# Kernel tuning notes

Hardware: AMD Instinct MI355X
Metric: run time of the kernel (lower is better)

The kernel has to match this reference:

```python
import jax, jax.numpy as jnp
import numpy as np

N = 10000      # nodes
E = 160000     # edges (before self loops)
F_IN = 512     # in_features
F_OUT = 256    # out_features
SLOPE = 0.2    # LeakyReLU negative slope (PyG GATConv default)
EPS = 1e-12    # F.normalize eps


def setup_inputs() -> dict:
    key = jax.random.key(0)
    ks = jax.random.split(key, 14)
    feat = jax.random.normal(ks[0], (N, F_IN), jnp.float32)
    feat_a = jax.random.normal(ks[1], (N, F_IN), jnp.float32)
    edge_index = jax.random.randint(ks[2], (2, E), 0, N, dtype=jnp.int32)
    # binary neighborhood mask; diagonal set so every row has >=1 entry
    gn = (jax.random.uniform(ks[3], (N, N)) < 0.0016).astype(jnp.float32)
    graph_neigh = gn.at[jnp.arange(N), jnp.arange(N)].set(1.0)
    s1 = 1.0 / np.sqrt(F_IN)
    s2 = 1.0 / np.sqrt(F_OUT)
    return {
        "feat": feat,
        "feat_a": feat_a,
        "edge_index": edge_index,
        "graph_neigh": graph_neigh,
        # conv1: GATConv(F_IN -> F_OUT, heads=1)
        "W1": jax.random.normal(ks[4], (F_OUT, F_IN), jnp.float32) * s1,
        "att_src1": jax.random.normal(ks[5], (F_OUT,), jnp.float32) * s2,
        "att_dst1": jax.random.normal(ks[6], (F_OUT,), jnp.float32) * s2,
        "b1": jnp.zeros((F_OUT,), jnp.float32),
        # conv2: GATConv(F_OUT -> F_IN, heads=1)
        "W2": jax.random.normal(ks[7], (F_IN, F_OUT), jnp.float32) * s2,
        "att_src2": jax.random.normal(ks[8], (F_IN,), jnp.float32) * s1,
        "att_dst2": jax.random.normal(ks[9], (F_IN,), jnp.float32) * s1,
        "b2": jnp.zeros((F_IN,), jnp.float32),
        # discriminator bilinear
        "Wd": jax.random.normal(ks[10], (F_OUT, F_OUT), jnp.float32) * s2,
        "bd": jnp.zeros((), jnp.float32),
    }


def _gat_conv(x, src, dst, W, a_src, a_dst, b):
    # PyG GATConv, heads=1, concat=True, add_self_loops already applied.
    h = x @ W.T                       # [N, out]
    a_s = h @ a_src                   # [N]
    a_d = h @ a_dst                   # [N]
    e = a_s[src] + a_d[dst]           # [E+N]
    e = jnp.where(e > 0, e, SLOPE * e)  # leaky relu
    m = jax.ops.segment_max(e, dst, num_segments=N)
    p = jnp.exp(e - m[dst])
    s = jax.ops.segment_sum(p, dst, num_segments=N)
    coef = p / s[dst]                 # per-dst softmax over incoming edges
    out = jax.ops.segment_sum(coef[:, None] * h[src], dst, num_segments=N)
    return out + b


def reference(feat, feat_a, edge_index, graph_neigh, W1, att_src1, att_dst1, b1,
              W2, att_src2, att_dst2, b2, Wd, bd):
    loops = jnp.arange(N, dtype=edge_index.dtype)
    src = jnp.concatenate([edge_index[0], loops])
    dst = jnp.concatenate([edge_index[1], loops])

    z = _gat_conv(feat, src, dst, W1, att_src1, att_dst1, b1)      # [N, F_OUT]
    hiden_emb = z
    h = _gat_conv(z, src, dst, W2, att_src2, att_dst2, b2)         # [N, F_IN]
    emb = jax.nn.relu(z)
    z_a = _gat_conv(feat_a, src, dst, W1, att_src1, att_dst1, b1)
    emb_a = jax.nn.relu(z_a)

    def readout(e):
        vsum = graph_neigh @ e                                     # [N, F_OUT]
        row_sum = graph_neigh.sum(axis=1, keepdims=True)
        g = vsum / row_sum
        g = g / jnp.maximum(jnp.linalg.norm(g, axis=1, keepdims=True), EPS)
        return jax.nn.sigmoid(g)

    g = readout(emb)
    g_a = readout(emb_a)

    def bilin(x1, x2):
        return jnp.einsum('nd,de,ne->n', x1, Wd, x2)[:, None] + bd

    ret = jnp.concatenate([bilin(emb, g), bilin(emb_a, g)], axis=1)      # [N, 2]
    ret_a = jnp.concatenate([bilin(emb_a, g_a), bilin(emb, g_a)], axis=1)
    return (hiden_emb, h, ret, ret_a)
```

## Files before the change

kernel.cpp:

```cpp
#include <hip/hip_runtime.h>


#define N_NODES 10000
#define F_IN    512
#define F_OUT   256
#define SLOPE   0.2f
#define BCAP    64

typedef unsigned short ushort_t;
typedef __attribute__((ext_vector_type(8))) short short8;
typedef __attribute__((ext_vector_type(4))) float f32x4;

__device__ __forceinline__ float bf2f(ushort_t h) {
    union { unsigned u; float f; } v;
    v.u = ((unsigned)h) << 16;
    return v.f;
}
__device__ __forceinline__ ushort_t f2bf(float f) {
    union { float f; unsigned u; } v; v.f = f;
    unsigned r = v.u + 0x7FFFu + ((v.u >> 16) & 1u);
    return (ushort_t)(r >> 16);
}

#define NF (N_NODES * 512)
#define NW1 (512 * 256)
#define NW2 (512 * 256)
#define NWD (256 * 256)

__global__ __launch_bounds__(256) void cvt_all(const float* __restrict__ feat,
                                               const float* __restrict__ feat_a,
                                               const float* __restrict__ W1,
                                               const float* __restrict__ W2,
                                               const float* __restrict__ Wd,
                                               ushort_t* __restrict__ featbf,
                                               ushort_t* __restrict__ W1bf,
                                               ushort_t* __restrict__ W2bf,
                                               ushort_t* __restrict__ Wdbf,
                                               uint4* __restrict__ zbase, int zu4) {
    int q = blockIdx.x * 256 + threadIdx.x;
    const int total = (2 * NF + NW1 + NW2 + NWD) / 4;
    if (q >= total) {
        int zi = q - total;
        if (zi < zu4) zbase[zi] = make_uint4(0, 0, 0, 0);
        return;
    }
    int i = q * 4;
    const float* s; ushort_t* d;
    if (i < NF)               { s = feat   + i;                 d = featbf + i; }
    else if (i < 2 * NF)      { s = feat_a + (i - NF);          d = featbf + i; }
    else if (i < 2 * NF + NW1){ s = W1 + (i - 2 * NF);          d = W1bf + (i - 2 * NF); }
    else if (i < 2 * NF + NW1 + NW2) { s = W2 + (i - 2 * NF - NW1); d = W2bf + (i - 2 * NF - NW1); }
    else                      { s = Wd + (i - 2 * NF - NW1 - NW2); d = Wdbf + (i - 2 * NF - NW1 - NW2); }
    float4 v = *(const float4*)s;
    uint2 r;
    r.x = (unsigned)f2bf(v.x) | ((unsigned)f2bf(v.y) << 16);
    r.y = (unsigned)f2bf(v.z) | ((unsigned)f2bf(v.w) << 16);
    *(uint2*)d = r;
}

#define BM 64
#define BN 64
#define BK 32
#define MT1 157
#define MT2 313

__device__ __forceinline__ void gemm_bt_dev(ushort_t* As, ushort_t* Bs,
        int bx, int by,
        const ushort_t* __restrict__ A, const ushort_t* __restrict__ B,
        ushort_t* __restrict__ C, int M, int Nn, int K,
        const float* __restrict__ asrc, const float* __restrict__ adst,
        float* __restrict__ as_out, float* __restrict__ ad_out) {
    int m0 = bx * BM;
    int n0 = by * BN;
    int tid = threadIdx.x;
    int wave = tid >> 6, lane = tid & 63;
    int quad = lane >> 4, r16 = lane & 15;

    f32x4 acc[4] = {};

    int srow = tid >> 2;
    int schunk = tid & 3;
    int a_row = m0 + srow; if (a_row >= M) a_row = M - 1;
    int swz = (schunk ^ (srow & 3)) * 8;
    const ushort_t* Ag = A + (size_t)a_row * K + swz;
    const ushort_t* Bg = B + (size_t)(n0 + srow) * K + swz;
#if __has_builtin(__builtin_amdgcn_global_load_lds)
    ushort_t* dA = As + wave * 512;
    ushort_t* dB = Bs + wave * 512;
#endif

    for (int k0 = 0; k0 < K; k0 += BK) {
#if __has_builtin(__builtin_amdgcn_global_load_lds)
        __syncthreads();
        __builtin_amdgcn_global_load_lds(
            (const __attribute__((address_space(1))) void*)(Ag + k0),
            (__attribute__((address_space(3))) void*)dA, 16, 0, 0);
        __builtin_amdgcn_global_load_lds(
            (const __attribute__((address_space(1))) void*)(Bg + k0),
            (__attribute__((address_space(3))) void*)dB, 16, 0, 0);
        __syncthreads();
#else
        uint4 av = *(const uint4*)(Ag + k0);
        uint4 bv = *(const uint4*)(Bg + k0);
        __syncthreads();
        *(uint4*)&As[srow * BK + ((schunk ^ (srow & 3)) * 8)] = av;
        *(uint4*)&Bs[srow * BK + ((schunk ^ (srow & 3)) * 8)] = bv;
        __syncthreads();
#endif
        int am = wave * 16 + r16;
        short8 a = *(const short8*)&As[am * BK + ((quad ^ (am & 3)) * 8)];
#pragma unroll
        for (int i = 0; i < 4; i++) {
            int bn = i * 16 + r16;
            short8 b = *(const short8*)&Bs[bn * BK + ((quad ^ (bn & 3)) * 8)];
            acc[i] = __builtin_amdgcn_mfma_f32_16x16x32_bf16(a, b, acc[i], 0, 0, 0);
        }
    }
    int m_base = m0 + wave * 16 + quad * 4;
#pragma unroll
    for (int i = 0; i < 4; i++) {
        int n = n0 + i * 16 + r16;
#pragma unroll
        for (int r = 0; r < 4; r++) {
            int m = m_base + r;
            if (m < M) C[(size_t)m * Nn + n] = f2bf(acc[i][r]);
        }
    }
    if (as_out) {
        float a0 = asrc[n0 + r16],      d0 = adst[n0 + r16];
        float a1 = asrc[n0 + 16 + r16], d1 = adst[n0 + 16 + r16];
        float a2 = asrc[n0 + 32 + r16], d2 = adst[n0 + 32 + r16];
        float a3 = asrc[n0 + 48 + r16], d3 = adst[n0 + 48 + r16];
#pragma unroll
        for (int r = 0; r < 4; r++) {
            float s  = acc[0][r] * a0 + acc[1][r] * a1 + acc[2][r] * a2 + acc[3][r] * a3;
            float dd = acc[0][r] * d0 + acc[1][r] * d1 + acc[2][r] * d2 + acc[3][r] * d3;
#pragma unroll
            for (int off = 1; off < 16; off <<= 1) {
                s  += __shfl_xor(s, off);
                dd += __shfl_xor(dd, off);
            }
            int m = m_base + r;
            if (r16 == 0 && m < M) {
                atomicAdd(&as_out[m], s);
                atomicAdd(&ad_out[m], dd);
            }
        }
    }
}

template<int NV>
__device__ __forceinline__ void accum_row(float wgt, const ushort_t* p, float* acc) {
    if constexpr (NV == 4) {
        uint2 u = *(const uint2*)p;
        acc[0] += wgt * bf2f((ushort_t)(u.x & 0xFFFFu));
        acc[1] += wgt * bf2f((ushort_t)(u.x >> 16));
        acc[2] += wgt * bf2f((ushort_t)(u.y & 0xFFFFu));
        acc[3] += wgt * bf2f((ushort_t)(u.y >> 16));
    } else {
        uint4 u = *(const uint4*)p;
        acc[0] += wgt * bf2f((ushort_t)(u.x & 0xFFFFu));
        acc[1] += wgt * bf2f((ushort_t)(u.x >> 16));
        acc[2] += wgt * bf2f((ushort_t)(u.y & 0xFFFFu));
        acc[3] += wgt * bf2f((ushort_t)(u.y >> 16));
        acc[4] += wgt * bf2f((ushort_t)(u.z & 0xFFFFu));
        acc[5] += wgt * bf2f((ushort_t)(u.z >> 16));
        acc[6] += wgt * bf2f((ushort_t)(u.w & 0xFFFFu));
        acc[7] += wgt * bf2f((ushort_t)(u.w >> 16));
    }
}

template<int NV>
__device__ __forceinline__ void store_bf(ushort_t* dst, const float* z, bool relu) {
    unsigned rp[NV / 2];
#pragma unroll
    for (int k = 0; k < NV; k += 2) {
        float x = relu ? fmaxf(z[k], 0.f) : z[k];
        float y = relu ? fmaxf(z[k + 1], 0.f) : z[k + 1];
        rp[k / 2] = (unsigned)f2bf(x) | ((unsigned)f2bf(y) << 16);
    }
    if constexpr (NV == 4) {
        *(uint2*)dst = make_uint2(rp[0], rp[1]);
    } else {
        *(uint4*)dst = make_uint4(rp[0], rp[1], rp[2], rp[3]);
    }
}

template<int FF>
__device__ __forceinline__ void row_conv_dev(int w,
        const int* __restrict__ cnt, const int* __restrict__ buckets,
        const float* __restrict__ a_s, const float* __restrict__ a_d,
        const ushort_t* __restrict__ h, const float* __restrict__ bias,
        int nfirst,
        float* __restrict__ out0, ushort_t* __restrict__ outZ,
        ushort_t* __restrict__ outB, ushort_t* __restrict__ out1) {
    constexpr int NV = FF / 64;
    int lane = threadIdx.x & 63;
    int sel = (w >= nfirst) ? 1 : 0;
    int n = w - sel * nfirst;
    size_t roff = (size_t)sel * (size_t)nfirst;
    int deg = min(cnt[n], BCAP);
    float adn = a_d[roff + n];

    float acc[NV];
#pragma unroll
    for (int k = 0; k < NV; k++) acc[k] = 0.f;

    int cv = 0; float e = -1e30f;
    if (lane < deg) {
        cv = buckets[n * BCAP + lane];
        float t = a_s[roff + cv] + adn;
        e = t > 0.f ? t : SLOPE * t;
    }
    float m = e;
#pragma unroll
    for (int off = 32; off; off >>= 1) m = fmaxf(m, __shfl_xor(m, off));
    float wv = (lane < deg) ? expf(e - m) : 0.f;
    float ls = wv;
#pragma unroll
    for (int off = 32; off; off >>= 1) ls += __shfl_xor(ls, off);
    float inv_s = ls > 0.f ? 1.f / ls : 0.f;
    int j = 0;
    for (; j + 3 < deg; j += 4) {
        float w0 = __shfl(wv, j),     w1 = __shfl(wv, j + 1);
        float w2 = __shfl(wv, j + 2), w3 = __shfl(wv, j + 3);
        int   q0 = __shfl(cv, j),     q1 = __shfl(cv, j + 1);
        int   q2 = __shfl(cv, j + 2), q3 = __shfl(cv, j + 3);
        accum_row<NV>(w0, h + (size_t)(roff + q0) * FF + lane * NV, acc);
        accum_row<NV>(w1, h + (size_t)(roff + q1) * FF + lane * NV, acc);
        accum_row<NV>(w2, h + (size_t)(roff + q2) * FF + lane * NV, acc);
        accum_row<NV>(w3, h + (size_t)(roff + q3) * FF + lane * NV, acc);
    }
    for (; j < deg; j++) {
        float wj = __shfl(wv, j);
        int   qj = __shfl(cv, j);
        accum_row<NV>(wj, h + (size_t)(roff + qj) * FF + lane * NV, acc);
    }

    float z[NV];
#pragma unroll
    for (int k = 0; k < NV; k++) z[k] = acc[k] * inv_s + bias[lane * NV + k];

    size_t obase = (size_t)n * FF + lane * NV;
    if (sel == 0) {
        if (out0) {
#pragma unroll
            for (int k = 0; k < NV; k += 4)
                *(float4*)(out0 + obase + k) = make_float4(z[k], z[k+1], z[k+2], z[k+3]);
        }
        if (outZ) store_bf<NV>(outZ + obase, z, false);
        if (outB) store_bf<NV>(outB + obase, z, true);
    } else {
        if (out1) store_bf<NV>(out1 + obase, z, true);
    }
}

template<int FF>
__global__ __launch_bounds__(256) void row_conv_w(const int* __restrict__ cnt,
                                                  const int* __restrict__ buckets,
                                                  const float* __restrict__ a_s,
                                                  const float* __restrict__ a_d,
                                                  const ushort_t* __restrict__ h,
                                                  const float* __restrict__ bias,
                                                  int nfirst, int ntot,
                                                  float* __restrict__ out0,
                                                  ushort_t* __restrict__ outZ,
                                                  ushort_t* __restrict__ outB,
                                                  ushort_t* __restrict__ out1) {
    int w = blockIdx.x * 4 + (threadIdx.x >> 6);
    if (w >= ntot) return;
    row_conv_dev<FF>(w, cnt, buckets, a_s, a_d, h, bias, nfirst, out0, outZ, outB, out1);
}

#define RCAP 256

__device__ __forceinline__ void readout_dev(int nbase, char* smemraw,
        const float* __restrict__ gn,
        const ushort_t* __restrict__ embB, const ushort_t* __restrict__ embA,
        ushort_t* __restrict__ g, ushort_t* __restrict__ ga) {
    int wid = threadIdx.x >> 6, lane = threadIdx.x & 63;
    int n = nbase + wid;
    int (*lists)[RCAP] = (int(*)[RCAP])smemraw;
    int* cnts = (int*)(smemraw + 4 * RCAP * 4);
    if (lane == 0) cnts[wid] = 0;
    __syncthreads();
    const uint4* rowp = (const uint4*)(gn + (size_t)n * N_NODES);
    const int NU4 = N_NODES / 4;
    for (int idx = lane; idx < NU4; idx += 64) {
        uint4 v = rowp[idx];
        if (v.x & 0x7FFFFFFFu) { int p = atomicAdd(&cnts[wid], 1); if (p < RCAP) lists[wid][p] = idx * 4; }
        if (v.y & 0x7FFFFFFFu) { int p = atomicAdd(&cnts[wid], 1); if (p < RCAP) lists[wid][p] = idx * 4 + 1; }
        if (v.z & 0x7FFFFFFFu) { int p = atomicAdd(&cnts[wid], 1); if (p < RCAP) lists[wid][p] = idx * 4 + 2; }
        if (v.w & 0x7FFFFFFFu) { int p = atomicAdd(&cnts[wid], 1); if (p < RCAP) lists[wid][p] = idx * 4 + 3; }
    }
    __syncthreads();
    int c = min(cnts[wid], RCAP);
    float a0[4] = {}, a1[4] = {};
    int j = 0;
    for (; j + 3 < c; j += 4) {
        int i0 = lists[wid][j],     i1 = lists[wid][j + 1];
        int i2 = lists[wid][j + 2], i3 = lists[wid][j + 3];
        accum_row<4>(1.f, embB + (size_t)i0 * 256 + lane * 4, a0);
        accum_row<4>(1.f, embB + (size_t)i1 * 256 + lane * 4, a0);
        accum_row<4>(1.f, embB + (size_t)i2 * 256 + lane * 4, a0);
        accum_row<4>(1.f, embB + (size_t)i3 * 256 + lane * 4, a0);
        accum_row<4>(1.f, embA + (size_t)i0 * 256 + lane * 4, a1);
        accum_row<4>(1.f, embA + (size_t)i1 * 256 + lane * 4, a1);
        accum_row<4>(1.f, embA + (size_t)i2 * 256 + lane * 4, a1);
        accum_row<4>(1.f, embA + (size_t)i3 * 256 + lane * 4, a1);
    }
    for (; j < c; j++) {
        int node = lists[wid][j];
        accum_row<4>(1.f, embB + (size_t)node * 256 + lane * 4, a0);
        accum_row<4>(1.f, embA + (size_t)node * 256 + lane * 4, a1);
    }
    float inv = 1.f / (float)(c > 0 ? c : 1);
    float u0[4], u1[4];
    float s0 = 0.f, s1 = 0.f;
#pragma unroll
    for (int k = 0; k < 4; k++) {
        u0[k] = a0[k] * inv; s0 += u0[k] * u0[k];
        u1[k] = a1[k] * inv; s1 += u1[k] * u1[k];
    }
#pragma unroll
    for (int off = 32; off; off >>= 1) {
        s0 += __shfl_xor(s0, off);
        s1 += __shfl_xor(s1, off);
    }
    float r0 = 1.f / fmaxf(sqrtf(s0), 1e-12f);
    float r1 = 1.f / fmaxf(sqrtf(s1), 1e-12f);
    float go[4], gao[4];
#pragma unroll
    for (int k = 0; k < 4; k++) {
        go[k]  = 1.f / (1.f + expf(-u0[k] * r0));
        gao[k] = 1.f / (1.f + expf(-u1[k] * r1));
    }
    store_bf<4>(g  + (size_t)n * 256 + lane * 4, go,  false);
    store_bf<4>(ga + (size_t)n * 256 + lane * 4, gao, false);
}

#define G1B (MT2 * 4)

__global__ __launch_bounds__(256) void k_conv1(const ushort_t* __restrict__ featbf,
                                               const ushort_t* __restrict__ W1bf,
                                               ushort_t* __restrict__ h1cat,
                                               const float* __restrict__ asrc1,
                                               const float* __restrict__ adst1,
                                               float* __restrict__ as1cat,
                                               float* __restrict__ ad1cat,
                                               const int* __restrict__ src,
                                               const int* __restrict__ dst,
                                               int E, int* cnt, int* buckets) {
    __shared__ __align__(16) ushort_t As[BM * BK];
    __shared__ __align__(16) ushort_t Bs[BN * BK];
    int b = blockIdx.x;
    if (b < G1B) {
        gemm_bt_dev(As, Bs, b % MT2, b / MT2, featbf, W1bf, h1cat,
                    2 * N_NODES, F_OUT, F_IN, asrc1, adst1, as1cat, ad1cat);
    } else {
        int i = (b - G1B) * 256 + (int)threadIdx.x;
        if (i < E) {
            int d = dst[i];
            d = d < 0 ? 0 : (d >= N_NODES ? N_NODES - 1 : d);
            int s = src[i];
            s = s < 0 ? 0 : (s >= N_NODES ? N_NODES - 1 : s);
            int p = atomicAdd(&cnt[d], 1);
            if (p < BCAP) buckets[d * BCAP + p] = s;
        } else if (i < E + N_NODES) {
            int v = i - E;
            int p = atomicAdd(&cnt[v], 1);
            if (p < BCAP) buckets[v * BCAP + p] = v;
        }
    }
}

#define RO_BLOCKS 2500
#define G2B (MT1 * 8)

__global__ __launch_bounds__(256) void k_stage2(const ushort_t* __restrict__ zbf,
                                                const ushort_t* __restrict__ W2bf,
                                                ushort_t* __restrict__ h2,
                                                const float* __restrict__ asrc2,
                                                const float* __restrict__ adst2,
                                                float* __restrict__ as2,
                                                float* __restrict__ ad2,
                                                const float* __restrict__ gn,
                                                const ushort_t* __restrict__ embB,
                                                const ushort_t* __restrict__ embA,
                                                ushort_t* __restrict__ g,
                                                ushort_t* __restrict__ ga) {
    __shared__ __align__(16) char smem[2 * BM * BK * 2];
    int b = blockIdx.x;
    if (b < RO_BLOCKS) {
        readout_dev(b * 4, smem, gn, embB, embA, g, ga);
    } else {
        int bb = b - RO_BLOCKS;
        gemm_bt_dev((ushort_t*)smem, (ushort_t*)smem + BM * BK, bb % MT1, bb / MT1,
                    zbf, W2bf, h2, N_NODES, F_IN, F_OUT, asrc2, adst2, as2, ad2);
    }
}

__global__ __launch_bounds__(256) void k_stage3(const int* __restrict__ cnt,
                                                const int* __restrict__ buckets,
                                                const float* __restrict__ as2,
                                                const float* __restrict__ ad2,
                                                const ushort_t* __restrict__ h2,
                                                const float* __restrict__ b2,
                                                float* __restrict__ out_h,
                                                const ushort_t* __restrict__ Gcat,
                                                const ushort_t* __restrict__ Wdbf,
                                                ushort_t* __restrict__ R2) {
    __shared__ __align__(16) ushort_t As[BM * BK];
    __shared__ __align__(16) ushort_t Bs[BN * BK];
    int b = blockIdx.x;
    if (b < RO_BLOCKS) {
        int w = b * 4 + ((int)threadIdx.x >> 6);
        row_conv_dev<512>(w, cnt, buckets, as2, ad2, h2, b2, N_NODES,
                          out_h, nullptr, nullptr, nullptr);
    } else {
        int bb = b - RO_BLOCKS;
        gemm_bt_dev(As, Bs, bb % MT2, bb / MT2, Gcat, Wdbf, R2,
                    2 * N_NODES, 256, 256, nullptr, nullptr, nullptr, nullptr);
    }
}

__global__ __launch_bounds__(256) void bilin_kernel(const float* __restrict__ z,
                                                    const ushort_t* __restrict__ embA,
                                                    const ushort_t* __restrict__ Q,
                                                    const ushort_t* __restrict__ Qa,
                                                    const float* __restrict__ bdp,
                                                    float* __restrict__ ret,
                                                    float* __restrict__ ret_a) {
    int row = blockIdx.x * 4 + (threadIdx.x >> 6);
    int lane = threadIdx.x & 63;
    if (row >= N_NODES) return;
    const float*    zr = z    + (size_t)row * 256;
    const ushort_t* er = embA + (size_t)row * 256;
    const ushort_t* q  = Q    + (size_t)row * 256;
    const ushort_t* qa = Qa   + (size_t)row * 256;
    float d00 = 0, d01 = 0, d10 = 0, d11 = 0;
    for (int d = lane; d < 256; d += 64) {
        float em = fmaxf(zr[d], 0.f);
        float ea = bf2f(er[d]);
        float qv = bf2f(q[d]), qav = bf2f(qa[d]);
        d00 += em * qv;
        d01 += ea * qv;
        d10 += ea * qav;
        d11 += em * qav;
    }
    for (int off = 32; off; off >>= 1) {
        d00 += __shfl_down(d00, off);
        d01 += __shfl_down(d01, off);
        d10 += __shfl_down(d10, off);
        d11 += __shfl_down(d11, off);
    }
    if (lane == 0) {
        float bd = bdp[0];
        ret[row * 2]       = d00 + bd;
        ret[row * 2 + 1]   = d01 + bd;
        ret_a[row * 2]     = d10 + bd;
        ret_a[row * 2 + 1] = d11 + bd;
    }
}

extern "C" void kernel_launch(void* const* d_in, const int* in_sizes, int n_in,
                              void* d_out, int out_size, void* d_ws, size_t ws_size,
                              hipStream_t stream) {
    const float* feat    = (const float*)d_in[0];
    const float* feat_a  = (const float*)d_in[1];
    const int*   eidx    = (const int*)d_in[2];
    const float* gn      = (const float*)d_in[3];
    const float* W1      = (const float*)d_in[4];
    const float* asrc1   = (const float*)d_in[5];
    const float* adst1   = (const float*)d_in[6];
    const float* b1      = (const float*)d_in[7];
    const float* W2      = (const float*)d_in[8];
    const float* asrc2   = (const float*)d_in[9];
    const float* adst2   = (const float*)d_in[10];
    const float* b2      = (const float*)d_in[11];
    const float* Wd      = (const float*)d_in[12];
    const float* bd      = (const float*)d_in[13];

    const int N = N_NODES;
    const int E = in_sizes[2] / 2;
    const int* src = eidx;
    const int* dst = eidx + E;

    float* out_z    = (float*)d_out;
    float* out_h    = out_z + (size_t)N * F_OUT;
    float* out_ret  = out_h + (size_t)N * F_IN;
    float* out_reta = out_ret + (size_t)N * 2;

    size_t off = 0;
    char* wsb = (char*)d_ws;
    auto carve = [&](size_t bytes) -> void* {
        void* p = wsb + off;
        off = (off + bytes + 255) & ~(size_t)255;
        return p;
    };
    ushort_t* R1     = (ushort_t*)carve((size_t)2 * N * 256 * 2);
    ushort_t* R2     = (ushort_t*)carve((size_t)2 * N * 256 * 2);
    ushort_t* Gcat   = (ushort_t*)carve((size_t)2 * N * 256 * 2);
    ushort_t* embA   = (ushort_t*)carve((size_t)N * 256 * 2);
    ushort_t* embB   = (ushort_t*)carve((size_t)N * 256 * 2);
    ushort_t* zbf    = (ushort_t*)carve((size_t)N * 256 * 2);
    ushort_t* featbf = (ushort_t*)carve((size_t)2 * N * 512 * 2);
    ushort_t* W1bf   = (ushort_t*)carve((size_t)NW1 * 2);
    ushort_t* W2bf   = (ushort_t*)carve((size_t)NW2 * 2);
    ushort_t* Wdbf   = (ushort_t*)carve((size_t)NWD * 2);
    size_t zstart = off;
    float* as1cat = (float*)carve((size_t)2 * N * 4);
    float* ad1cat = (float*)carve((size_t)2 * N * 4);
    float* as2    = (float*)carve((size_t)N * 4);
    float* ad2    = (float*)carve((size_t)N * 4);
    int*   cnt    = (int*)carve((size_t)N * 4);
    size_t zend = off;
    int*   buckets = (int*)carve((size_t)N * BCAP * 4);

    ushort_t* h1cat = R1;
    ushort_t* h2    = R1;
    ushort_t* Qb    = R2;
    ushort_t* Qab   = R2 + (size_t)N * 256;

    const int cvt_total = (2 * NF + NW1 + NW2 + NWD) / 4;
    const int zu4 = (int)((zend - zstart) / 16);
    cvt_all<<<(cvt_total + zu4 + 255) / 256, 256, 0, stream>>>(
        feat, feat_a, W1, W2, Wd, featbf, W1bf, W2bf, Wdbf,
        (uint4*)(wsb + zstart), zu4);

    const int bucketBlocks = (E + N + 255) / 256;
    k_conv1<<<G1B + bucketBlocks, 256, 0, stream>>>(featbf, W1bf, h1cat,
                                                    asrc1, adst1, as1cat, ad1cat,
                                                    src, dst, E, cnt, buckets);

    row_conv_w<256><<<2 * N / 4, 256, 0, stream>>>(cnt, buckets, as1cat, ad1cat, h1cat, b1,
                                                   N, 2 * N, out_z, zbf, embB, embA);

    k_stage2<<<RO_BLOCKS + G2B, 256, 0, stream>>>(zbf, W2bf, h2, asrc2, adst2, as2, ad2,
                                                  gn, embB, embA, Gcat, Gcat + (size_t)N * 256);

    k_stage3<<<RO_BLOCKS + G1B, 256, 0, stream>>>(cnt, buckets, as2, ad2, h2, b2, out_h,
                                                  Gcat, Wdbf, R2);

    bilin_kernel<<<(N + 3) / 4, 256, 0, stream>>>(out_z, embA, Qb, Qab, bd, out_ret, out_reta);
}
```

Measured before the change: 682.9 us.

## Fuse bilinear discriminator into Wd GEMM epilogue and drop bilin kernel

Result: no change. 679.1 us (-0.6%).

```diff
diff --git a/kernel.cpp b/kernel.cpp
--- a/kernel.cpp
+++ b/kernel.cpp
@@ -36,12 +36,15 @@
                                                ushort_t* __restrict__ W1bf,
                                                ushort_t* __restrict__ W2bf,
                                                ushort_t* __restrict__ Wdbf,
-                                               uint4* __restrict__ zbase, int zu4) {
+                                               uint4* __restrict__ zbase, int zu4,
+                                               uint4* __restrict__ zbase2, int zu4b) {
     int q = blockIdx.x * 256 + threadIdx.x;
     const int total = (2 * NF + NW1 + NW2 + NWD) / 4;
     if (q >= total) {
         int zi = q - total;
-        if (zi < zu4) zbase[zi] = make_uint4(0, 0, 0, 0);
+        if (zi < zu4) { zbase[zi] = make_uint4(0, 0, 0, 0); return; }
+        int zi2 = zi - zu4;
+        if (zi2 < zu4b) zbase2[zi2] = make_uint4(0, 0, 0, 0);
         return;
     }
     int i = q * 4;
@@ -69,7 +72,13 @@
         const ushort_t* __restrict__ A, const ushort_t* __restrict__ B,
         ushort_t* __restrict__ C, int M, int Nn, int K,
         const float* __restrict__ asrc, const float* __restrict__ adst,
-        float* __restrict__ as_out, float* __restrict__ ad_out) {
+        float* __restrict__ as_out, float* __restrict__ ad_out,
+        const ushort_t* __restrict__ embB_ = nullptr,
+        const ushort_t* __restrict__ embA_ = nullptr,
+        float* __restrict__ ret = nullptr,
+        float* __restrict__ ret_a = nullptr,
+        const float* __restrict__ bdp = nullptr,
+        int nfirst = 0) {
     int m0 = bx * BM;
     int n0 = by * BN;
     int tid = threadIdx.x;
@@ -117,13 +126,15 @@
         }
     }
     int m_base = m0 + wave * 16 + quad * 4;
-#pragma unroll
-    for (int i = 0; i < 4; i++) {
-        int n = n0 + i * 16 + r16;
-#pragma unroll
-        for (int r = 0; r < 4; r++) {
-            int m = m_base + r;
-            if (m < M) C[(size_t)m * Nn + n] = f2bf(acc[i][r]);
+    if (C) {
+#pragma unroll
+        for (int i = 0; i < 4; i++) {
+            int n = n0 + i * 16 + r16;
+#pragma unroll
+            for (int r = 0; r < 4; r++) {
+                int m = m_base + r;
+                if (m < M) C[(size_t)m * Nn + n] = f2bf(acc[i][r]);
+            }
         }
     }
     if (as_out) {
@@ -144,6 +155,37 @@
             if (r16 == 0 && m < M) {
                 atomicAdd(&as_out[m], s);
                 atomicAdd(&ad_out[m], dd);
+            }
+        }
+    }
+    if (ret) {
+        float bd = (n0 == 0) ? bdp[0] : 0.f;
+#pragma unroll
+        for (int r = 0; r < 4; r++) {
+            int m = m_base + r;
+            int isA = (m >= nfirst) ? 1 : 0;
+            int mm = m - isA * nfirst;
+            float db = 0.f, da = 0.f;
+#pragma unroll
+            for (int i = 0; i < 4; i++) {
+                int c = n0 + i * 16 + r16;
+                float qv = acc[i][r];
+                db += qv * bf2f(embB_[(size_t)mm * 256 + c]);
+                da += qv * bf2f(embA_[(size_t)mm * 256 + c]);
+            }
+#pragma unroll
+            for (int off = 1; off < 16; off <<= 1) {
+                db += __shfl_xor(db, off);
+                da += __shfl_xor(da, off);
+            }
+            if (r16 == 0 && m < M) {
+                if (!isA) {
+                    atomicAdd(&ret[mm * 2],     db + bd);
+                    atomicAdd(&ret[mm * 2 + 1], da + bd);
+                } else {
+                    atomicAdd(&ret_a[mm * 2],     da + bd);
+                    atomicAdd(&ret_a[mm * 2 + 1], db + bd);
+                }
             }
         }
     }
@@ -409,7 +451,11 @@
                                                 float* __restrict__ out_h,
                                                 const ushort_t* __restrict__ Gcat,
                                                 const ushort_t* __restrict__ Wdbf,
-                                                ushort_t* __restrict__ R2) {
+                                                const ushort_t* __restrict__ embB,
+                                                const ushort_t* __restrict__ embA,
+                                                float* __restrict__ ret,
+                                                float* __restrict__ ret_a,
+                                                const float* __restrict__ bdp) {
     __shared__ __align__(16) ushort_t As[BM * BK];
     __shared__ __align__(16) ushort_t Bs[BN * BK];
     int b = blockIdx.x;
@@ -419,47 +465,9 @@
                           out_h, nullptr, nullptr, nullptr);
     } else {
         int bb = b - RO_BLOCKS;
-        gemm_bt_dev(As, Bs, bb % MT2, bb / MT2, Gcat, Wdbf, R2,
-                    2 * N_NODES, 256, 256, nullptr, nullptr, nullptr, nullptr);
-    }
-}
-
-__global__ __launch_bounds__(256) void bilin_kernel(const float* __restrict__ z,
-                                                    const ushort_t* __restrict__ embA,
-                                                    const ushort_t* __restrict__ Q,
-                                                    const ushort_t* __restrict__ Qa,
-                                                    const float* __restrict__ bdp,
-                                                    float* __restrict__ ret,
-                                                    float* __restrict__ ret_a) {
-    int row = blockIdx.x * 4 + (threadIdx.x >> 6);
-    int lane = threadIdx.x & 63;
-    if (row >= N_NODES) return;
-    const float*    zr = z    + (size_t)row * 256;
-    const ushort_t* er = embA + (size_t)row * 256;
-    const ushort_t* q  = Q    + (size_t)row * 256;
-    const ushort_t* qa = Qa   + (size_t)row * 256;
-    float d00 = 0, d01 = 0, d10 = 0, d11 = 0;
-    for (int d = lane; d < 256; d += 64) {
-        float em = fmaxf(zr[d], 0.f);
-        float ea = bf2f(er[d]);
-        float qv = bf2f(q[d]), qav = bf2f(qa[d]);
-        d00 += em * qv;
-        d01 += ea * qv;
-        d10 += ea * qav;
-        d11 += em * qav;
-    }
-    for (int off = 32; off; off >>= 1) {
-        d00 += __shfl_down(d00, off);
-        d01 += __shfl_down(d01, off);
-        d10 += __shfl_down(d10, off);
-        d11 += __shfl_down(d11, off);
-    }
-    if (lane == 0) {
-        float bd = bdp[0];
-        ret[row * 2]       = d00 + bd;
-        ret[row * 2 + 1]   = d01 + bd;
-        ret_a[row * 2]     = d10 + bd;
-        ret_a[row * 2 + 1] = d11 + bd;
+        gemm_bt_dev(As, Bs, bb % MT2, bb / MT2, Gcat, Wdbf, nullptr,
+                    2 * N_NODES, 256, 256, nullptr, nullptr, nullptr, nullptr,
+                    embB, embA, ret, ret_a, bdp, N_NODES);
     }
 }
 
@@ -499,7 +507,6 @@
         return p;
     };
     ushort_t* R1     = (ushort_t*)carve((size_t)2 * N * 256 * 2);
-    ushort_t* R2     = (ushort_t*)carve((size_t)2 * N * 256 * 2);
     ushort_t* Gcat   = (ushort_t*)carve((size_t)2 * N * 256 * 2);
     ushort_t* embA   = (ushort_t*)carve((size_t)N * 256 * 2);
     ushort_t* embB   = (ushort_t*)carve((size_t)N * 256 * 2);
@@ -519,14 +526,13 @@
 
     ushort_t* h1cat = R1;
     ushort_t* h2    = R1;
-    ushort_t* Qb    = R2;
-    ushort_t* Qab   = R2 + (size_t)N * 256;
 
     const int cvt_total = (2 * NF + NW1 + NW2 + NWD) / 4;
     const int zu4 = (int)((zend - zstart) / 16);
-    cvt_all<<<(cvt_total + zu4 + 255) / 256, 256, 0, stream>>>(
+    const int zu4b = (int)((size_t)N * 4 * 4 / 16);
+    cvt_all<<<(cvt_total + zu4 + zu4b + 255) / 256, 256, 0, stream>>>(
         feat, feat_a, W1, W2, Wd, featbf, W1bf, W2bf, Wdbf,
-        (uint4*)(wsb + zstart), zu4);
+        (uint4*)(wsb + zstart), zu4, (uint4*)out_ret, zu4b);
 
     const int bucketBlocks = (E + N + 255) / 256;
     k_conv1<<<G1B + bucketBlocks, 256, 0, stream>>>(featbf, W1bf, h1cat,
@@ -540,7 +546,6 @@
                                                   gn, embB, embA, Gcat, Gcat + (size_t)N * 256);
 
     k_stage3<<<RO_BLOCKS + G1B, 256, 0, stream>>>(cnt, buckets, as2, ad2, h2, b2, out_h,
-                                                  Gcat, Wdbf, R2);
-
-    bilin_kernel<<<(N + 3) / 4, 256, 0, stream>>>(out_z, embA, Qb, Qab, bd, out_ret, out_reta);
-}
+                                                  Gcat, Wdbf, embB, embA,
+                                                  out_ret, out_reta, bd);
+}
```
